# Performance work log

Hardware: AMD Instinct MI355X
Metric: run time of the kernel (lower is better)

The kernel has to match this reference:

```python
import jax, jax.numpy as jnp
import numpy as np

B, T, C, H, N_LAYER, LAYER_ID = 4, 2048, 1024, 16, 12, 6
N = C // H
Q = 256  # T % 256 == 0 -> chunk size used by the module


def setup_inputs():
    key = jax.random.key(0)
    ks = jax.random.split(key, 9)
    r0 = LAYER_ID / (N_LAYER - 1)
    r1 = 1.0 - LAYER_ID / N_LAYER
    ddd = (jnp.arange(C, dtype=jnp.float32) / C)[None, None, :]
    h = jnp.arange(C, dtype=jnp.float32)
    s = 1.0 / np.sqrt(C)
    return {
        "x": jax.random.normal(ks[0], (B, T, C), jnp.float32),
        "time_maa_x": 1.0 - ddd ** r1,
        "time_maa_w": 1.0 - ddd ** r1,
        "time_maa_k": 1.0 - ddd ** r1,
        "time_maa_v": 1.0 - (ddd ** r1 + 0.3 * r0),
        "time_maa_r": 1.0 - ddd ** (0.5 * r1),
        "maa_w1": jax.random.uniform(ks[1], (C, 4 * 32), jnp.float32, minval=-0.01, maxval=0.01),
        "maa_w2": jax.random.uniform(ks[2], (4, 32, C), jnp.float32, minval=-0.01, maxval=0.01),
        "decay_w1": jax.random.uniform(ks[3], (C, 64), jnp.float32, minval=-0.01, maxval=0.01),
        "decay_w2": jax.random.uniform(ks[4], (64, C), jnp.float32, minval=-0.01, maxval=0.01),
        "time_decay": (-6.0 + 5.0 * (h / (C - 1)) ** (0.7 + 1.3 * r0))[None, None, :],
        "time_faaaa": (r0 * (1.0 - h / (C - 1))).reshape(1, H, 1, 1, N),
        "Wr": jax.random.normal(ks[5], (C, C), jnp.float32) * s,
        "Wk": jax.random.normal(ks[6], (C, C), jnp.float32) * s,
        "Wv": jax.random.normal(ks[7], (C, C), jnp.float32) * s,
        "Wo": jax.random.normal(ks[8], (C, C), jnp.float32) * s,
        "ln_g": jnp.ones((C,), jnp.float32),
        "ln_b": jnp.zeros((C,), jnp.float32),
    }


def _forward(x, time_maa_x, time_maa_w, time_maa_k, time_maa_v, time_maa_r,
             maa_w1, maa_w2, decay_w1, decay_w2, time_decay, time_faaaa,
             Wr, Wk, Wv, Wo, ln_g, ln_b):
    b, t, c = x.shape
    nc = t // Q
    # time_shift: zero-pad one step at front of time axis, drop last step
    xx = jnp.pad(x, ((0, 0), (1, 0), (0, 0)))[:, :-1] - x
    xxx = x + xx * time_maa_x
    m = jnp.tanh(xxx @ maa_w1).reshape(b, t, 4, -1)  # [B,T,4,32]
    m = jnp.einsum('btfd,fdc->fbtc', m, maa_w2)       # [4,B,T,C]
    mw, mk, mv, mr = m[0], m[1], m[2], m[3]
    xw = x + xx * (time_maa_w + mw)
    xk = x + xx * (time_maa_k + mk)
    xv = x + xx * (time_maa_v + mv)
    xr = x + xx * (time_maa_r + mr)
    r = (xr @ Wr).reshape(b, t, H, N).transpose(0, 2, 1, 3)  # [B,H,T,N]
    k = (xk @ Wk).reshape(b, t, H, N).transpose(0, 2, 1, 3)
    v = (xv @ Wv).reshape(b, t, H, N).transpose(0, 2, 1, 3)
    w = time_decay + jnp.tanh(xw @ decay_w1) @ decay_w2      # [B,T,C]
    w = w.reshape(b, t, H, N).transpose(0, 2, 1, 3).mean(axis=-1)  # [B,H,T]
    w_log = -jnp.exp(w)
    wc = w_log.reshape(b, H, nc, Q, 1)
    wc_cum = jnp.cumsum(wc, axis=-2)
    shifted = jnp.pad(wc_cum, ((0, 0), (0, 0), (0, 0), (1, 0), (0, 0)))[..., :-1, :]
    ws_log = wc.sum(axis=-2, keepdims=True)   # [B,H,nc,1,1]
    w_inter = jnp.exp(ws_log - wc_cum)        # [B,H,nc,Q,1]
    w_intra = jnp.exp(wc_cum - wc)            # [B,H,nc,Q,1]
    ws = jnp.exp(ws_log)                      # [B,H,nc,1,1]
    A = shifted - jnp.swapaxes(wc_cum, -1, -2)  # [B,H,nc,Q,Q]
    strict = jnp.tril(jnp.ones((Q, Q), dtype=bool), -1)
    # torch: tril() -> exp() -> tril(-1)  ==  exp on strict-lower, zero elsewhere
    w_mask = jnp.where(strict, jnp.exp(jnp.where(strict, A, 0.0)), 0.0)
    rr = r.reshape(b, H, nc, Q, N)
    kk = k.reshape(b, H, nc, Q, N)
    vv = v.reshape(b, H, nc, Q, N)
    kv = jnp.einsum('bhcqn,bhcqm->bhcnm', kk * w_inter, vv)  # [B,H,nc,N,N]

    def step(state, inp):
        ws_i, kv_i = inp
        return ws_i * state + kv_i, state  # emit state BEFORE update (as in torch loop)

    _, states = jax.lax.scan(step, jnp.zeros((b, H, N, N), x.dtype),
                             (jnp.moveaxis(ws, 2, 0), jnp.moveaxis(kv, 2, 0)))
    states = jnp.moveaxis(states, 0, 2)  # [B,H,nc,N,N]
    inter = jnp.einsum('bhcqn,bhcnm->bhcqm', rr * w_intra, states)
    scores = jnp.einsum('bhcqn,bhckn->bhcqk', rr, kk) * w_mask
    diag = jnp.sum(rr * (time_faaaa * kk), axis=-1)  # [B,H,nc,Q]
    intra = jnp.einsum('bhcqk,bhckm->bhcqm', scores, vv) + diag[..., None] * vv
    y = (inter + intra).reshape(b, H, t, N).transpose(0, 2, 1, 3).reshape(b, t, c)
    mu = y.mean(axis=-1, keepdims=True)
    var = ((y - mu) ** 2).mean(axis=-1, keepdims=True)
    y = (y - mu) / jnp.sqrt(var + 1e-5) * ln_g + ln_b  # ln_x
    return y @ Wo  # output projection (dropout p=0)


def reference(x, time_maa_x, time_maa_w, time_maa_k, time_maa_v, time_maa_r,
              maa_w1, maa_w2, decay_w1, decay_w2, time_decay, time_faaaa,
              Wr, Wk, Wv, Wo, ln_g, ln_b):
    return _forward(x, time_maa_x, time_maa_w, time_maa_k, time_maa_v, time_maa_r,
                    maa_w1, maa_w2, decay_w1, decay_w2, time_decay, time_faaaa,
                    Wr, Wk, Wv, Wo, ln_g, ln_b)
```

## Files before the change

### kernel.cpp

```cpp
#include <hip/hip_runtime.h>
#include <math.h>

#define BB 4
#define TT 2048
#define CC 1024
#define HH 16
#define NN 64
#define QQ 256
#define NCH 8
#define BT 8192

typedef unsigned short u16;
typedef __attribute__((ext_vector_type(8))) short bf16x8;
typedef __attribute__((ext_vector_type(4))) short bf16x4;
typedef __attribute__((ext_vector_type(4))) float f32x4;
typedef __attribute__((ext_vector_type(4))) u16 u16x4;

__device__ inline u16 f2b(float x) {
  union { float f; unsigned u; } v;
  v.f = x;
  unsigned r = v.u + 0x7FFFu + ((v.u >> 16) & 1u);
  return (u16)(r >> 16);
}
__device__ inline float b2f(u16 u) {
  union { unsigned u; float f; } v;
  v.u = ((unsigned)u) << 16;
  return v.f;
}
__device__ inline bf16x8 ldfrag(const u16* p) {
  bf16x4 lo = *(const bf16x4*)p;
  bf16x4 hi = *(const bf16x4*)(p + 4);
  return __builtin_shufflevector(lo, hi, 0, 1, 2, 3, 4, 5, 6, 7);
}
__device__ inline void stage_tile(const u16* __restrict__ g, size_t base,
                                  int pitch, int tid, u16* __restrict__ lds) {
#pragma unroll
  for (int it = 0; it < 2; it++) {
    int cidx = tid + it * 256;
    int r = cidx >> 3, c8 = (cidx & 7) * 8;
    bf16x8 v = *(const bf16x8*)(g + base + (size_t)r * pitch + c8);
    *(bf16x4*)(lds + r * 72 + c8) = __builtin_shufflevector(v, v, 0, 1, 2, 3);
    *(bf16x4*)(lds + r * 72 + c8 + 4) = __builtin_shufflevector(v, v, 4, 5, 6, 7);
  }
}

__global__ __launch_bounds__(256) void mix_kernel(const float* __restrict__ x,
                                                  const float* __restrict__ tmx,
                                                  float* __restrict__ xx,
                                                  u16* __restrict__ xxxb) {
  size_t e = ((size_t)blockIdx.x * 256 + threadIdx.x) * 4;
  int c = (int)(e & 1023);
  size_t row = e >> 10;
  int t = (int)(row & 2047);
  float4 xv = *(const float4*)(x + e);
  float4 pv = make_float4(0.f, 0.f, 0.f, 0.f);
  if (t > 0) pv = *(const float4*)(x + e - 1024);
  float4 d = make_float4(pv.x - xv.x, pv.y - xv.y, pv.z - xv.z, pv.w - xv.w);
  *(float4*)(xx + e) = d;
  u16x4 o;
  o.x = f2b(xv.x + d.x * tmx[c + 0]);
  o.y = f2b(xv.y + d.y * tmx[c + 1]);
  o.z = f2b(xv.z + d.z * tmx[c + 2]);
  o.w = f2b(xv.w + d.w * tmx[c + 3]);
  *(u16x4*)(xxxb + e) = o;
}

__global__ __launch_bounds__(256) void cvt_wT(const float* __restrict__ W0,
                                              const float* __restrict__ W1,
                                              const float* __restrict__ W2,
                                              const float* __restrict__ W3,
                                              u16* __restrict__ O0,
                                              u16* __restrict__ O1,
                                              u16* __restrict__ O2,
                                              u16* __restrict__ O3) {
  const float* W;
  u16* O;
  switch (blockIdx.z) {
    case 0: W = W0; O = O0; break;
    case 1: W = W1; O = O1; break;
    case 2: W = W2; O = O2; break;
    default: W = W3; O = O3; break;
  }
  __shared__ float t[64][65];
  int bx = blockIdx.x * 64;
  int by = blockIdx.y * 64;
#pragma unroll
  for (int it = 0; it < 16; it++) {
    int idx = it * 256 + threadIdx.x;
    int r = idx >> 6, c = idx & 63;
    t[r][c] = W[(size_t)(by + r) * 1024 + bx + c];
  }
  __syncthreads();
#pragma unroll
  for (int it = 0; it < 16; it++) {
    int idx = it * 256 + threadIdx.x;
    int n = idx >> 6, k = idx & 63;
    O[(size_t)(bx + n) * 1024 + by + k] = f2b(t[k][n]);
  }
}

__global__ __launch_bounds__(256) void cvt_T(const float* __restrict__ in,
                                             u16* __restrict__ out, int R, int C) {
  __shared__ float t[64][65];
  int c0 = blockIdx.x * 64, r0 = blockIdx.y * 64;
#pragma unroll
  for (int it = 0; it < 16; it++) {
    int idx = it * 256 + threadIdx.x;
    int r = idx >> 6, c = idx & 63;
    t[r][c] = in[(size_t)(r0 + r) * C + c0 + c];
  }
  __syncthreads();
#pragma unroll
  for (int it = 0; it < 16; it++) {
    int idx = it * 256 + threadIdx.x;
    int c = idx >> 6, r = idx & 63;
    out[(size_t)(c0 + c) * R + r0 + r] = f2b(t[r][c]);
  }
}

template <bool TANH>
__global__ __launch_bounds__(256) void gemm_bt_mfma(const u16* __restrict__ A,
                                                    const u16* __restrict__ Bt,
                                                    float* __restrict__ Cf,
                                                    u16* __restrict__ Cb,
                                                    int M, int N, int K) {
  __shared__ u16 As[128 * 32];
  __shared__ u16 Bs[128 * 32];
  const int tid = threadIdx.x;
  const int lane = tid & 63;
  const int row0 = blockIdx.y * 128;
  const int col0 = blockIdx.x * 128;
  const int wave = tid >> 6;
  const int wr = (wave >> 1) * 64;
  const int wc = (wave & 1) * 64;
  const int fr = lane & 15;
  const int fq = lane >> 4;

  f32x4 acc[4][4];
#pragma unroll
  for (int i = 0; i < 4; i++)
#pragma unroll
    for (int j = 0; j < 4; j++) acc[i][j] = (f32x4){0.f, 0.f, 0.f, 0.f};

  const int i0 = tid, i1 = tid + 256;
  const int ra0 = i0 >> 2, ca0 = (i0 & 3) * 8;
  const int ra1 = i1 >> 2, ca1 = (i1 & 3) * 8;

  for (int k0 = 0; k0 < K; k0 += 32) {
    __builtin_amdgcn_global_load_lds(
        (const __attribute__((address_space(1))) void*)(A + (size_t)(row0 + ra0) * K + k0 + ca0),
        (__attribute__((address_space(3))) void*)(As + i0 * 8), 16, 0, 0);
    __builtin_amdgcn_global_load_lds(
        (const __attribute__((address_space(1))) void*)(A + (size_t)(row0 + ra1) * K + k0 + ca1),
        (__attribute__((address_space(3))) void*)(As + i1 * 8), 16, 0, 0);
    __builtin_amdgcn_global_load_lds(
        (const __attribute__((address_space(1))) void*)(Bt + (size_t)(col0 + ra0) * K + k0 + ca0),
        (__attribute__((address_space(3))) void*)(Bs + i0 * 8), 16, 0, 0);
    __builtin_amdgcn_global_load_lds(
        (const __attribute__((address_space(1))) void*)(Bt + (size_t)(col0 + ra1) * K + k0 + ca1),
        (__attribute__((address_space(3))) void*)(Bs + i1 * 8), 16, 0, 0);
    __syncthreads();

    bf16x8 af[4], bf[4];
#pragma unroll
    for (int i = 0; i < 4; i++)
      af[i] = *(const bf16x8*)(As + ((wr + i * 16 + fr) * 32 + fq * 8));
#pragma unroll
    for (int j = 0; j < 4; j++)
      bf[j] = *(const bf16x8*)(Bs + ((wc + j * 16 + fr) * 32 + fq * 8));
#pragma unroll
    for (int i = 0; i < 4; i++)
#pragma unroll
      for (int j = 0; j < 4; j++)
        acc[i][j] = __builtin_amdgcn_mfma_f32_16x16x32_bf16(af[i], bf[j], acc[i][j], 0, 0, 0);
    __syncthreads();
  }
#pragma unroll
  for (int i = 0; i < 4; i++) {
    int grow = row0 + wr + i * 16 + fq * 4;
#pragma unroll
    for (int j = 0; j < 4; j++) {
      int gcol = col0 + wc + j * 16 + fr;
#pragma unroll
      for (int r = 0; r < 4; r++) {
        float vv = acc[i][j][r];
        if (TANH) vv = tanhf(vv);
        if (Cf) Cf[(size_t)(grow + r) * N + gcol] = vv;
        if (Cb) Cb[(size_t)(grow + r) * N + gcol] = f2b(vv);
      }
    }
  }
}

#define DP_ABUF 8192
#define DP_BBUF 16384
#define DP_SBUF 24576
#define DP_SMEM_BYTES 147456

template <bool TRIPLE, bool F32OUT>
__global__ __launch_bounds__(512, 2) void gemm_dp(
    const u16* __restrict__ A0, const u16* __restrict__ A1,
    const u16* __restrict__ A2, const u16* __restrict__ B0,
    const u16* __restrict__ B1, const u16* __restrict__ B2,
    float* __restrict__ Cf, u16* __restrict__ C0, u16* __restrict__ C1,
    u16* __restrict__ C2) {
  extern __shared__ __align__(16) u16 smem[];
  const int nwg = (int)(gridDim.x * gridDim.y * gridDim.z);
  const int wg = (int)(blockIdx.x + (blockIdx.y << 2) + (blockIdx.z << 8));
  const int cpx = nwg >> 3;
  const int swz = (wg & 7) * cpx + (wg >> 3);
  const int bx = swz & 3;
  const int by = (swz >> 2) & 63;
  const int bz = swz >> 8;

  const u16* __restrict__ A;
  const u16* __restrict__ Bt;
  u16* __restrict__ Cb;
  if (TRIPLE) {
    switch (bz) {
      case 0: A = A0; Bt = B0; Cb = C0; break;
      case 1: A = A1; Bt = B1; Cb = C1; break;
      default: A = A2; Bt = B2; Cb = C2; break;
    }
  } else {
    A = A0; Bt = B0; Cb = C0;
  }

  const int tid = threadIdx.x;
  const int lane = tid & 63;
  const int wave = tid >> 6;
  const int wr = (wave >> 2) * 64;
  const int wc = (wave & 3) * 64;
  const int fr = lane & 15;
  const int fq = lane >> 4;
  const int s8 = fr & 7;
  const int row0 = by * 128;
  const int col0 = bx * 256;

  int aoff[4][2], boff[4][2];
#pragma unroll
  for (int mi = 0; mi < 4; mi++)
#pragma unroll
    for (int ks = 0; ks < 2; ks++)
      aoff[mi][ks] = (wr + mi * 16 + fr) * 64 + (((ks * 4 + fq) ^ s8) * 8);
#pragma unroll
  for (int nj = 0; nj < 4; nj++)
#pragma unroll
    for (int ks = 0; ks < 2; ks++)
      boff[nj][ks] = (wc + nj * 16 + fr) * 64 + (((ks * 4 + fq) ^ s8) * 8);

  auto stage = [&](int kt, int q) {
    const u16* __restrict__ gA = A + (size_t)row0 * 1024 + kt * 64;
    const u16* __restrict__ gB = Bt + (size_t)col0 * 1024 + kt * 64;
    u16* dA = smem + q * DP_SBUF;
    u16* dB = dA + DP_ABUF;
#pragma unroll
    for (int p = 0; p < 2; p++) {
      int pos = tid + p * 512;
      int r = pos >> 3, gch = (pos & 7) ^ (r & 7);
      __builtin_amdgcn_global_load_lds(
          (const __attribute__((address_space(1))) void*)(gA + (size_t)r * 1024 + gch * 8),
          (__attribute__((address_space(3))) void*)(dA + pos * 8), 16, 0, 0);
    }
#pragma unroll
    for (int p = 0; p < 4; p++) {
      int pos = tid + p * 512;
      int r = pos >> 3, gch = (pos & 7) ^ (r & 7);
      __builtin_amdgcn_global_load_lds(
          (const __attribute__((address_space(1))) void*)(gB + (size_t)r * 1024 + gch * 8),
          (__attribute__((address_space(3))) void*)(dB + pos * 8), 16, 0, 0);
    }
  };

  f32x4 acc[4][4];
#pragma unroll
  for (int mi = 0; mi < 4; mi++)
#pragma unroll
    for (int nj = 0; nj < 4; nj++) acc[mi][nj] = (f32x4){0.f, 0.f, 0.f, 0.f};

  auto iter_body = [&](int qc, int qs, bool dostage, int t2) {
    if (dostage) stage(t2, qs);
    const u16* sA = smem + qc * DP_SBUF;
    const u16* sB = sA + DP_ABUF;
    bf16x8 av[4][2], bv[4][2];
#pragma unroll
    for (int mi = 0; mi < 4; mi++)
#pragma unroll
      for (int ks = 0; ks < 2; ks++)
        av[mi][ks] = *(const bf16x8*)(sA + aoff[mi][ks]);
#pragma unroll
    for (int nj = 0; nj < 4; nj++)
#pragma unroll
      for (int ks = 0; ks < 2; ks++)
        bv[nj][ks] = *(const bf16x8*)(sB + boff[nj][ks]);
    __builtin_amdgcn_s_setprio(1);
#pragma unroll
    for (int ks = 0; ks < 2; ks++)
#pragma unroll
      for (int mi = 0; mi < 4; mi++)
#pragma unroll
        for (int nj = 0; nj < 4; nj++)
          acc[mi][nj] = __builtin_amdgcn_mfma_f32_16x16x32_bf16(
              av[mi][ks], bv[nj][ks], acc[mi][nj], 0, 0, 0);
    __builtin_amdgcn_s_setprio(0);
  };

  stage(0, 0);
  stage(1, 1);
  int qc = 0, qs = 2;
  for (int t = 0; t < 14; t++) {
    asm volatile("s_waitcnt vmcnt(6)" ::: "memory");
    __builtin_amdgcn_s_barrier();
    iter_body(qc, qs, true, t + 2);
    qc = (qc == 2) ? 0 : qc + 1;
    qs = (qs == 2) ? 0 : qs + 1;
  }
  asm volatile("s_waitcnt vmcnt(6)" ::: "memory");
  __builtin_amdgcn_s_barrier();
  iter_body(qc, 0, false, 0);
  qc = (qc == 2) ? 0 : qc + 1;
  asm volatile("s_waitcnt vmcnt(0)" ::: "memory");
  __builtin_amdgcn_s_barrier();
  iter_body(qc, 0, false, 0);

#pragma unroll
  for (int mi = 0; mi < 4; mi++) {
    int grow = row0 + wr + mi * 16 + fq * 4;
#pragma unroll
    for (int nj = 0; nj < 4; nj++) {
      int gcol = col0 + wc + nj * 16 + fr;
#pragma unroll
      for (int r = 0; r < 4; r++) {
        if (F32OUT)
          Cf[(size_t)(grow + r) * 1024 + gcol] = acc[mi][nj][r];
        else
          Cb[(size_t)(grow + r) * 1024 + gcol] = f2b(acc[mi][nj][r]);
      }
    }
  }
}

__global__ __launch_bounds__(256) void blend_mfma(
    const u16* __restrict__ mb, const u16* __restrict__ w2T,
    const float* __restrict__ x, const float* __restrict__ xx,
    const float* __restrict__ tmw, const float* __restrict__ tmk,
    const float* __restrict__ tmv, const float* __restrict__ tmr,
    u16* __restrict__ xwb, u16* __restrict__ xkb, u16* __restrict__ xvb,
    u16* __restrict__ xrb) {
  __shared__ u16 mS[64 * 136];
  __shared__ u16 wS[64 * 136];
  const int tid = threadIdx.x;
  const int lane = tid & 63;
  const int w = tid >> 6;
  const int fr = lane & 15;
  const int fq = lane >> 4;
  const int c0 = blockIdx.x * 64;
  const int bt0 = blockIdx.y * 64;

#pragma unroll
  for (int it = 0; it < 4; it++) {
    int idx = tid + it * 256;
    int r = idx >> 4, c8 = (idx & 15) * 8;
    bf16x8 v = *(const bf16x8*)(mb + (size_t)(bt0 + r) * 128 + c8);
    *(bf16x4*)(mS + r * 136 + c8) = __builtin_shufflevector(v, v, 0, 1, 2, 3);
    *(bf16x4*)(mS + r * 136 + c8 + 4) = __builtin_shufflevector(v, v, 4, 5, 6, 7);
    bf16x8 u = *(const bf16x8*)(w2T + (size_t)(c0 + r) * 128 + c8);
    *(bf16x4*)(wS + r * 136 + c8) = __builtin_shufflevector(u, u, 0, 1, 2, 3);
    *(bf16x4*)(wS + r * 136 + c8 + 4) = __builtin_shufflevector(u, u, 4, 5, 6, 7);
  }
  __syncthreads();

  f32x4 acc[4][4];
#pragma unroll
  for (int j = 0; j < 4; j++)
#pragma unroll
    for (int f = 0; f < 4; f++) acc[j][f] = (f32x4){0.f, 0.f, 0.f, 0.f};

#pragma unroll
  for (int f = 0; f < 4; f++) {
    bf16x8 aA = ldfrag(mS + (w * 16 + fr) * 136 + f * 32 + fq * 8);
#pragma unroll
    for (int j = 0; j < 4; j++) {
      bf16x8 bB = ldfrag(wS + (j * 16 + fr) * 136 + f * 32 + fq * 8);
      acc[j][f] = __builtin_amdgcn_mfma_f32_16x16x32_bf16(aA, bB, acc[j][f], 0, 0, 0);
    }
  }

#pragma unroll
  for (int j = 0; j < 4; j++) {
    int c = c0 + j * 16 + fr;
    float w_ = tmw[c], k_ = tmk[c], v_ = tmv[c], r_ = tmr[c];
#pragma unroll
    for (int rr = 0; rr < 4; rr++) {
      int bt = bt0 + w * 16 + fq * 4 + rr;
      size_t g = (size_t)bt * 1024 + c;
      float xv_ = x[g], dx = xx[g];
      xwb[g] = f2b(xv_ + dx * (w_ + acc[j][0][rr]));
      xkb[g] = f2b(xv_ + dx * (k_ + acc[j][1][rr]));
      xvb[g] = f2b(xv_ + dx * (v_ + acc[j][2][rr]));
      xrb[g] = f2b(xv_ + dx * (r_ + acc[j][3][rr]));
    }
  }
}

__global__ __launch_bounds__(256) void dw2r_kernel(const float* __restrict__ dw2,
                                                   const float* __restrict__ td,
                                                   float* __restrict__ dw2r,
                                                   float* __restrict__ tdr,
                                                   u16* __restrict__ dw2rbT) {
  int idx = blockIdx.x * 256 + threadIdx.x;
  if (idx < 1024) {
    int j = idx >> 4, h = idx & 15;
    float s = 0.f;
    for (int n = 0; n < 64; n++) s += dw2[(size_t)j * 1024 + h * 64 + n];
    float m = s * (1.f / 64.f);
    dw2r[j * 16 + h] = m;
    dw2rbT[h * 64 + j] = f2b(m);
  }
  if (idx < 16) {
    float s = 0.f;
    for (int n = 0; n < 64; n++) s += td[idx * 64 + n];
    tdr[idx] = s * (1.f / 64.f);
  }
}

__global__ __launch_bounds__(256) void decay_mfma(const u16* __restrict__ xwb,
                                                  const u16* __restrict__ d1T,
                                                  const u16* __restrict__ dw2rbT,
                                                  const float* __restrict__ tdr,
                                                  float* __restrict__ wlog) {
  __shared__ u16 As[64 * 32];
  __shared__ u16 Bs[64 * 32];
  __shared__ u16 h1S[64 * 72];
  __shared__ u16 dwS[16 * 72];
  const int tid = threadIdx.x;
  const int lane = tid & 63;
  const int w = tid >> 6;
  const int fr = lane & 15;
  const int fq = lane >> 4;
  const int bt0 = blockIdx.x * 64;

#pragma unroll
  for (int it = 0; it < 4; it++) {
    int idx = tid + it * 256;
    int r = idx >> 6, c = idx & 63;
    dwS[r * 72 + c] = dw2rbT[r * 64 + c];
  }

  f32x4 acc[4];
#pragma unroll
  for (int j = 0; j < 4; j++) acc[j] = (f32x4){0.f, 0.f, 0.f, 0.f};

  const int ra = tid >> 2, ca = (tid & 3) * 8;
  for (int k0 = 0; k0 < 1024; k0 += 32) {
    __builtin_amdgcn_global_load_lds(
        (const __attribute__((address_space(1))) void*)(xwb + (size_t)(bt0 + ra) * 1024 + k0 + ca),
        (__attribute__((address_space(3))) void*)(As + tid * 8), 16, 0, 0);
    __builtin_amdgcn_global_load_lds(
        (const __attribute__((address_space(1))) void*)(d1T + (size_t)ra * 1024 + k0 + ca),
        (__attribute__((address_space(3))) void*)(Bs + tid * 8), 16, 0, 0);
    __syncthreads();
    bf16x8 aA = *(const bf16x8*)(As + ((w * 16 + fr) * 32 + fq * 8));
#pragma unroll
    for (int j = 0; j < 4; j++) {
      bf16x8 bB = *(const bf16x8*)(Bs + ((j * 16 + fr) * 32 + fq * 8));
      acc[j] = __builtin_amdgcn_mfma_f32_16x16x32_bf16(aA, bB, acc[j], 0, 0, 0);
    }
    __syncthreads();
  }
#pragma unroll
  for (int j = 0; j < 4; j++)
#pragma unroll
    for (int rr = 0; rr < 4; rr++)
      h1S[(w * 16 + fq * 4 + rr) * 72 + j * 16 + fr] = f2b(tanhf(acc[j][rr]));
  __syncthreads();

  f32x4 a2 = (f32x4){0.f, 0.f, 0.f, 0.f};
#pragma unroll
  for (int ks = 0; ks < 2; ks++) {
    bf16x8 aA = ldfrag(h1S + (w * 16 + fr) * 72 + ks * 32 + fq * 8);
    bf16x8 bB = ldfrag(dwS + fr * 72 + ks * 32 + fq * 8);
    a2 = __builtin_amdgcn_mfma_f32_16x16x32_bf16(aA, bB, a2, 0, 0, 0);
  }
  float tdv = tdr[fr];
#pragma unroll
  for (int rr = 0; rr < 4; rr++) {
    int bt = bt0 + w * 16 + fq * 4 + rr;
    int b = bt >> 11, tl = bt & 2047;
    wlog[((size_t)(b * 16 + fr)) * 2048 + tl] = -__expf(tdv + a2[rr]);
  }
}

__global__ __launch_bounds__(256) void wprep_kernel(const float* __restrict__ wlog,
                                                    float* __restrict__ cum,
                                                    float* __restrict__ excl,
                                                    float* __restrict__ wsl) {
  int bid = blockIdx.x;
  int c = bid & 7, bh = bid >> 3;
  int q = threadIdx.x;
  float v = wlog[(size_t)bh * 2048 + c * 256 + q];
  __shared__ float s[256];
  s[q] = v;
  float val = v;
  for (int off = 1; off < 256; off <<= 1) {
    __syncthreads();
    float t = (q >= off) ? s[q - off] : 0.f;
    __syncthreads();
    val += t;
    s[q] = val;
  }
  __syncthreads();
  float total = s[255];
  cum[(size_t)bid * 256 + q] = val;
  excl[(size_t)bid * 256 + q] = val - v;
  if (q == 0) wsl[bid] = total;
}

__global__ __launch_bounds__(256) void kvtrans2_kernel(
    const u16* __restrict__ vb, const u16* __restrict__ kb,
    const u16* __restrict__ rb, const float* __restrict__ faaaa,
    const float* __restrict__ cum, const float* __restrict__ wsl,
    u16* __restrict__ vT, u16* __restrict__ kTw, float* __restrict__ diagG) {
  int tt = blockIdx.x;
  int bh = blockIdx.y;
  int b = bh >> 4, h = bh & 15;
  int cc = tt >> 2;
  int bidc = bh * 8 + cc;
  __shared__ float tv[64][65];
  __shared__ float tk[64][65];
  __shared__ float wfac[64];
  __shared__ float faS[64];
  const int tid = threadIdx.x;
  float wslog = wsl[bidc];
  if (tid < 64) {
    wfac[tid] = __expf(wslog - cum[(size_t)bidc * 256 + (tt & 3) * 64 + tid]);
    faS[tid] = faaaa[h * 64 + tid];
  }
  __syncthreads();
  const int m = tid & 63;
  float fam = faS[m];
#pragma unroll
  for (int it = 0; it < 16; it++) {
    int r = it * 4 + (tid >> 6);
    size_t g = ((size_t)(b * TT + tt * 64 + r)) * CC + h * 64 + m;
    float vraw = b2f(vb[g]);
    float kraw = b2f(kb[g]);
    float rraw = b2f(rb[g]);
    tv[r][m] = vraw;
    tk[r][m] = kraw;
    float s = rraw * fam * kraw;
    s += __shfl_xor(s, 1);
    s += __shfl_xor(s, 2);
    s += __shfl_xor(s, 4);
    s += __shfl_xor(s, 8);
    s += __shfl_xor(s, 16);
    s += __shfl_xor(s, 32);
    if (m == 0) diagG[(size_t)bh * 2048 + tt * 64 + r] = s;
  }
  __syncthreads();
#pragma unroll
  for (int it = 0; it < 16; it++) {
    int idx = it * 256 + tid;
    int mm = idx >> 6, tl = idx & 63;
    size_t o = ((size_t)(bh * 64 + mm)) * TT + tt * 64 + tl;
    vT[o] = f2b(tv[tl][mm]);
    kTw[o] = f2b(tk[tl][mm] * wfac[tl]);
  }
}

__global__ __launch_bounds__(256) void kv_mfma(const u16* __restrict__ kTw,
                                               const u16* __restrict__ vT,
                                               float* __restrict__ kvb) {
  int bid = blockIdx.x;
  int c = bid & 7, bh = bid >> 3;
  __shared__ u16 kS[64 * 72];
  __shared__ u16 vS[64 * 72];
  const int tid = threadIdx.x;
  const int lane = tid & 63;
  const int w = tid >> 6;
  const int fr = lane & 15;
  const int fq = lane >> 4;
  f32x4 acc[4];
#pragma unroll
  for (int j = 0; j < 4; j++) acc[j] = (f32x4){0.f, 0.f, 0.f, 0.f};
  const size_t base = (size_t)bh * 64 * TT + c * QQ;
  for (int qt = 0; qt < 4; qt++) {
    __syncthreads();
    stage_tile(kTw, base + qt * 64, TT, tid, kS);
    stage_tile(vT, base + qt * 64, TT, tid, vS);
    __syncthreads();
#pragma unroll
    for (int ks = 0; ks < 2; ks++) {
      bf16x8 aA = ldfrag(kS + (w * 16 + fr) * 72 + ks * 32 + fq * 8);
#pragma unroll
      for (int j = 0; j < 4; j++) {
        bf16x8 bB = ldfrag(vS + (j * 16 + fr) * 72 + ks * 32 + fq * 8);
        acc[j] = __builtin_amdgcn_mfma_f32_16x16x32_bf16(aA, bB, acc[j], 0, 0, 0);
      }
    }
  }
#pragma unroll
  for (int j = 0; j < 4; j++)
#pragma unroll
    for (int rr = 0; rr < 4; rr++)
      kvb[(size_t)bid * 4096 + (w * 16 + fq * 4 + rr) * 64 + j * 16 + fr] = acc[j][rr];
}

__global__ __launch_bounds__(256) void scan_kernel(const float* __restrict__ kvb,
                                                   const float* __restrict__ wsl,
                                                   float* __restrict__ st) {
  int bh = blockIdx.x;
  int tid = threadIdx.x;
  float s[16];
#pragma unroll
  for (int i = 0; i < 16; i++) s[i] = 0.f;
  for (int c = 0; c < 8; c++) {
    int bid = bh * 8 + c;
    float w = __expf(wsl[bid]);
#pragma unroll
    for (int i = 0; i < 16; i++) {
      size_t e = (size_t)bid * 4096 + i * 256 + tid;
      st[e] = s[i];
      s[i] = w * s[i] + kvb[e];
    }
  }
}

__global__ __launch_bounds__(256) void attn_mfma(
    const u16* __restrict__ rb, const u16* __restrict__ kb,
    const u16* __restrict__ vT, const float* __restrict__ stg,
    const float* __restrict__ cum, const float* __restrict__ excl,
    const float* __restrict__ diagG, float* __restrict__ y) {
  int bid = blockIdx.x;
  int c = bid & 7, bh = bid >> 3;
  int b = bh >> 4, h = bh & 15;
  __shared__ u16 rt[64 * 72];
  __shared__ u16 kt[64 * 72];
  __shared__ u16 vt[64 * 72];
  __shared__ u16 pt[64 * 72];
  __shared__ u16 stT[64 * 72];
  __shared__ float cumS[256], exS[256], diagS[256], ekS[256];

  const int tid = threadIdx.x;
  const int lane = tid & 63;
  const int w = tid >> 6;
  const int fr = lane & 15;
  const int fq = lane >> 4;

  cumS[tid] = cum[(size_t)bid * 256 + tid];
  exS[tid] = excl[(size_t)bid * 256 + tid];
  diagS[tid] = diagG[(size_t)bh * 2048 + c * 256 + tid];
#pragma unroll
  for (int it = 0; it < 16; it++) {
    int idx = tid + it * 256;
    int n = idx >> 6, mm = idx & 63;
    stT[mm * 72 + n] = f2b(stg[(size_t)bid * 4096 + idx]);
  }
  __syncthreads();
  const float ccm = cumS[127];
  ekS[tid] = __expf(ccm - cumS[tid]);

  const size_t rowbase = ((size_t)b * TT + c * QQ) * CC + h * 64;
  const size_t vbase0 = (size_t)bh * 64 * TT + c * QQ;

  for (int qt = 0; qt < 4; qt++) {
    __syncthreads();
    stage_tile(rb, rowbase + (size_t)(qt * 64) * CC, CC, tid, rt);
    __syncthreads();

    f32x4 acc[4];
#pragma unroll
    for (int jm = 0; jm < 4; jm++) acc[jm] = (f32x4){0.f, 0.f, 0.f, 0.f};
    bf16x8 rA[2];
    rA[0] = ldfrag(rt + (w * 16 + fr) * 72 + fq * 8);
    rA[1] = ldfrag(rt + (w * 16 + fr) * 72 + 32 + fq * 8);
#pragma unroll
    for (int ks = 0; ks < 2; ks++)
#pragma unroll
      for (int jm = 0; jm < 4; jm++) {
        bf16x8 bB = ldfrag(stT + (jm * 16 + fr) * 72 + ks * 32 + fq * 8);
        acc[jm] = __builtin_amdgcn_mfma_f32_16x16x32_bf16(rA[ks], bB, acc[jm], 0, 0, 0);
      }
    int ql0 = w * 16 + fq * 4;
    float er[4], eqc[4];
#pragma unroll
    for (int rr = 0; rr < 4; rr++) {
      float ex = exS[qt * 64 + ql0 + rr];
      er[rr] = __expf(ex);
      eqc[rr] = __expf(ex - ccm);
    }
#pragma unroll
    for (int jm = 0; jm < 4; jm++)
#pragma unroll
      for (int rr = 0; rr < 4; rr++) acc[jm][rr] *= er[rr];

    for (int kti = 0; kti <= qt; kti++) {
      __syncthreads();
      stage_tile(kb, rowbase + (size_t)(kti * 64) * CC, CC, tid, kt);
      stage_tile(vT, vbase0 + (size_t)(kti * 64), TT, tid, vt);
      __syncthreads();

      f32x4 sacc[4];
#pragma unroll
      for (int jj = 0; jj < 4; jj++) sacc[jj] = (f32x4){0.f, 0.f, 0.f, 0.f};
#pragma unroll
      for (int ks = 0; ks < 2; ks++)
#pragma unroll
        for (int jj = 0; jj < 4; jj++) {
          bf16x8 bB = ldfrag(kt + (jj * 16 + fr) * 72 + ks * 32 + fq * 8);
          sacc[jj] = __builtin_amdgcn_mfma_f32_16x16x32_bf16(rA[ks], bB, sacc[jj], 0, 0, 0);
        }
#pragma unroll
      for (int jj = 0; jj < 4; jj++) {
        int kcol = kti * 64 + jj * 16 + fr;
        float ek = ekS[kcol];
#pragma unroll
        for (int rr = 0; rr < 4; rr++) {
          int qrow = qt * 64 + ql0 + rr;
          float vsc;
          if (kcol < qrow)
            vsc = sacc[jj][rr] * eqc[rr] * ek;
          else if (kcol == qrow)
            vsc = diagS[qrow];
          else
            vsc = 0.f;
          pt[(ql0 + rr) * 72 + jj * 16 + fr] = f2b(vsc);
        }
      }
      __syncthreads();
#pragma unroll
      for (int ks = 0; ks < 2; ks++) {
        bf16x8 pA = ldfrag(pt + (w * 16 + fr) * 72 + ks * 32 + fq * 8);
#pragma unroll
        for (int jm = 0; jm < 4; jm++) {
          bf16x8 vB = ldfrag(vt + (jm * 16 + fr) * 72 + ks * 32 + fq * 8);
          acc[jm] = __builtin_amdgcn_mfma_f32_16x16x32_bf16(pA, vB, acc[jm], 0, 0, 0);
        }
      }
    }
    int qg0 = qt * 64 + w * 16 + fq * 4;
#pragma unroll
    for (int jm = 0; jm < 4; jm++)
#pragma unroll
      for (int rr = 0; rr < 4; rr++)
        y[rowbase + (size_t)(qg0 + rr) * CC + jm * 16 + fr] = acc[jm][rr];
  }
}

__global__ __launch_bounds__(256) void ln_kernel(const float* __restrict__ y,
                                                 const float* __restrict__ g,
                                                 const float* __restrict__ bta,
                                                 u16* __restrict__ out) {
  __shared__ float red[8];
  int bt = blockIdx.x;
  int tid = threadIdx.x;
  float v[4];
  float s = 0.f;
#pragma unroll
  for (int i = 0; i < 4; i++) {
    v[i] = y[(size_t)bt * 1024 + i * 256 + tid];
    s += v[i];
  }
#pragma unroll
  for (int off = 32; off > 0; off >>= 1) s += __shfl_down(s, off);
  if ((tid & 63) == 0) red[tid >> 6] = s;
  __syncthreads();
  if (tid == 0) red[4] = red[0] + red[1] + red[2] + red[3];
  __syncthreads();
  float mu = red[4] * (1.f / 1024.f);
  float s2 = 0.f;
#pragma unroll
  for (int i = 0; i < 4; i++) {
    float d = v[i] - mu;
    s2 += d * d;
  }
#pragma unroll
  for (int off = 32; off > 0; off >>= 1) s2 += __shfl_down(s2, off);
  __syncthreads();
  if ((tid & 63) == 0) red[tid >> 6] = s2;
  __syncthreads();
  if (tid == 0) red[5] = red[0] + red[1] + red[2] + red[3];
  __syncthreads();
  float var = red[5] * (1.f / 1024.f);
  float rstd = rsqrtf(var + 1e-5f);
#pragma unroll
  for (int i = 0; i < 4; i++) {
    int c = i * 256 + tid;
    out[(size_t)bt * 1024 + c] = f2b((v[i] - mu) * rstd * g[c] + bta[c]);
  }
}

extern "C" void kernel_launch(void* const* d_in, const int* in_sizes, int n_in,
                              void* d_out, int out_size, void* d_ws,
                              size_t ws_size, hipStream_t stream) {
  const float* x = (const float*)d_in[0];
  const float* tmx = (const float*)d_in[1];
  const float* tmw = (const float*)d_in[2];
  const float* tmk = (const float*)d_in[3];
  const float* tmv = (const float*)d_in[4];
  const float* tmr = (const float*)d_in[5];
  const float* maa_w1 = (const float*)d_in[6];
  const float* maa_w2 = (const float*)d_in[7];
  const float* decay_w1 = (const float*)d_in[8];
  const float* decay_w2 = (const float*)d_in[9];
  const float* time_decay = (const float*)d_in[10];
  const float* faaaa = (const float*)d_in[11];
  const float* Wr = (const float*)d_in[12];
  const float* Wk = (const float*)d_in[13];
  const float* Wv = (const float*)d_in[14];
  const float* Wo = (const float*)d_in[15];
  const float* lng = (const float*)d_in[16];
  const float* lnb = (const float*)d_in[17];
  float* out = (float*)d_out;
  float* ws = (float*)d_ws;

  const size_t S = (size_t)BT * CC;

  float* xx = ws;
  float* dw2r = ws + S;
  float* tdr = dw2r + 1024;
  float* wlog = tdr + 1024;
  float* cum = wlog + 131072;
  float* excl = cum + 131072;
  float* wsl = excl + 131072;
  float* diagG = wsl + 1024;
  float* kvb = diagG + 131072;
  float* stb = kvb + (size_t)512 * 4096;
  float* fend = stb + (size_t)512 * 4096;
  u16* xxxb = (u16*)fend;
  u16* mb = xxxb + S;
  u16* xkb = mb + (size_t)BT * 128;
  u16* xvb = xkb + S;
  u16* xrb = xvb + S;
  u16* xwb = xrb + S;
  u16* rb16 = xwb + S;
  u16* kb16 = rb16 + S;
  u16* Vb = kb16 + S;
  u16* Wrt = Vb + S;
  u16* Wkt = Wrt + (size_t)1024 * 1024;
  u16* Wvt = Wkt + (size_t)1024 * 1024;
  u16* Wot = Wvt + (size_t)1024 * 1024;
  u16* w1T = Wot + (size_t)1024 * 1024;
  u16* w2T = w1T + (size_t)128 * 1024;
  u16* d1T = w2T + (size_t)1024 * 128;
  u16* dw2rbT = d1T + (size_t)64 * 1024;
  u16* vT = xxxb;
  u16* kTw = xrb;
  float* y_ = xx;
  u16* ylnb = xkb;

  static bool attr_done = false;
  if (!attr_done) {
    hipFuncSetAttribute((const void*)gemm_dp<true, false>,
                        hipFuncAttributeMaxDynamicSharedMemorySize, DP_SMEM_BYTES);
    hipFuncSetAttribute((const void*)gemm_dp<false, true>,
                        hipFuncAttributeMaxDynamicSharedMemorySize, DP_SMEM_BYTES);
    attr_done = true;
  }

  cvt_wT<<<dim3(16, 16, 4), 256, 0, stream>>>(Wr, Wk, Wv, Wo, Wrt, Wkt, Wvt, Wot);
  cvt_T<<<dim3(2, 16), 256, 0, stream>>>(maa_w1, w1T, 1024, 128);
  cvt_T<<<dim3(16, 2), 256, 0, stream>>>(maa_w2, w2T, 128, 1024);
  cvt_T<<<dim3(1, 16), 256, 0, stream>>>(decay_w1, d1T, 1024, 64);
  dw2r_kernel<<<4, 256, 0, stream>>>(decay_w2, time_decay, dw2r, tdr, dw2rbT);
  mix_kernel<<<8192, 256, 0, stream>>>(x, tmx, xx, xxxb);
  gemm_bt_mfma<true><<<dim3(1, 64), 256, 0, stream>>>(xxxb, w1T, nullptr, mb, BT, 128, CC);
  blend_mfma<<<dim3(16, 128), 256, 0, stream>>>(mb, w2T, x, xx, tmw, tmk, tmv,
                                                tmr, xwb, xkb, xvb, xrb);
  decay_mfma<<<128, 256, 0, stream>>>(xwb, d1T, dw2rbT, tdr, wlog);
  wprep_kernel<<<512, 256, 0, stream>>>(wlog, cum, excl, wsl);
  gemm_dp<true, false><<<dim3(4, 64, 3), 512, DP_SMEM_BYTES, stream>>>(
      xrb, xkb, xvb, Wrt, Wkt, Wvt, nullptr, rb16, kb16, Vb);
  kvtrans2_kernel<<<dim3(32, 64), 256, 0, stream>>>(Vb, kb16, rb16, faaaa, cum,
                                                    wsl, vT, kTw, diagG);
  kv_mfma<<<512, 256, 0, stream>>>(kTw, vT, kvb);
  scan_kernel<<<64, 256, 0, stream>>>(kvb, wsl, stb);
  attn_mfma<<<512, 256, 0, stream>>>(rb16, kb16, vT, stb, cum, excl, diagG, y_);
  ln_kernel<<<BT, 256, 0, stream>>>(y_, lng, lnb, ylnb);
  gemm_dp<false, true><<<dim3(4, 64, 1), 512, DP_SMEM_BYTES, stream>>>(
      ylnb, nullptr, nullptr, Wot, nullptr, nullptr, out, nullptr, nullptr,
      nullptr);
}
```

Baseline: 378.5 us.

## Split GEMM k-tile into two ping-pong phases with interleaved staging and barriers

Restructures the gemm_dp main loop so each 64-wide k-tile runs as two half-phases. Each phase loads its LDS fragments, issues part of the next tile's global-to-LDS loads, waits on a barrier and lgkmcnt, then runs 16 MFMAs at raised priority. The aim is to interleave LDS reads, async global loads and MFMA work across the two waves per SIMD, in the style of a ping-pong schedule. The cost is twice as many workgroup barriers per tile and tighter coupling between waves. The vmcnt accounting also has to stay correct now that loads are split across two phases.

```diff
diff --git a/kernel.cpp b/kernel.cpp
--- a/kernel.cpp
+++ b/kernel.cpp
@@ -197,6 +197,11 @@
 #define DP_SBUF 24576
 #define DP_SMEM_BYTES 147456
 
+#define PE_PLAIN 0
+#define PE_VM6 1
+#define PE_VM0 2
+#define PE_NONE 3
+
 template <bool TRIPLE, bool F32OUT>
 __global__ __launch_bounds__(512, 2) void gemm_dp(
     const u16* __restrict__ A0, const u16* __restrict__ A1,
@@ -249,7 +254,7 @@
     for (int ks = 0; ks < 2; ks++)
       boff[nj][ks] = (wc + nj * 16 + fr) * 64 + (((ks * 4 + fq) ^ s8) * 8);
 
-  auto stage = [&](int kt, int q) {
+  auto stage_pA = [&](int kt, int q) {
     const u16* __restrict__ gA = A + (size_t)row0 * 1024 + kt * 64;
     const u16* __restrict__ gB = Bt + (size_t)col0 * 1024 + kt * 64;
     u16* dA = smem + q * DP_SBUF;
@@ -262,8 +267,19 @@
           (const __attribute__((address_space(1))) void*)(gA + (size_t)r * 1024 + gch * 8),
           (__attribute__((address_space(3))) void*)(dA + pos * 8), 16, 0, 0);
     }
-#pragma unroll
-    for (int p = 0; p < 4; p++) {
+    {
+      int pos = tid;
+      int r = pos >> 3, gch = (pos & 7) ^ (r & 7);
+      __builtin_amdgcn_global_load_lds(
+          (const __attribute__((address_space(1))) void*)(gB + (size_t)r * 1024 + gch * 8),
+          (__attribute__((address_space(3))) void*)(dB + pos * 8), 16, 0, 0);
+    }
+  };
+  auto stage_pB = [&](int kt, int q) {
+    const u16* __restrict__ gB = Bt + (size_t)col0 * 1024 + kt * 64;
+    u16* dB = smem + q * DP_SBUF + DP_ABUF;
+#pragma unroll
+    for (int p = 1; p < 4; p++) {
       int pos = tid + p * 512;
       int r = pos >> 3, gch = (pos & 7) ^ (r & 7);
       __builtin_amdgcn_global_load_lds(
@@ -278,50 +294,57 @@
 #pragma unroll
     for (int nj = 0; nj < 4; nj++) acc[mi][nj] = (f32x4){0.f, 0.f, 0.f, 0.f};
 
-  auto iter_body = [&](int qc, int qs, bool dostage, int t2) {
-    if (dostage) stage(t2, qs);
+  auto phase = [&](int qc, int ks, int dostage, int t2, int qs, int pe) {
     const u16* sA = smem + qc * DP_SBUF;
     const u16* sB = sA + DP_ABUF;
-    bf16x8 av[4][2], bv[4][2];
+    bf16x8 av[4], bv[4];
+#pragma unroll
+    for (int mi = 0; mi < 4; mi++) av[mi] = *(const bf16x8*)(sA + aoff[mi][ks]);
+#pragma unroll
+    for (int nj = 0; nj < 4; nj++) bv[nj] = *(const bf16x8*)(sB + boff[nj][ks]);
+    if (dostage == 1) stage_pA(t2, qs);
+    else if (dostage == 2) stage_pB(t2, qs);
+    __builtin_amdgcn_s_barrier();
+    asm volatile("s_waitcnt lgkmcnt(0)" ::: "memory");
+    __builtin_amdgcn_sched_barrier(0);
+    __builtin_amdgcn_s_setprio(1);
 #pragma unroll
     for (int mi = 0; mi < 4; mi++)
 #pragma unroll
-      for (int ks = 0; ks < 2; ks++)
-        av[mi][ks] = *(const bf16x8*)(sA + aoff[mi][ks]);
-#pragma unroll
-    for (int nj = 0; nj < 4; nj++)
-#pragma unroll
-      for (int ks = 0; ks < 2; ks++)
-        bv[nj][ks] = *(const bf16x8*)(sB + boff[nj][ks]);
-    __builtin_amdgcn_s_setprio(1);
-#pragma unroll
-    for (int ks = 0; ks < 2; ks++)
-#pragma unroll
-      for (int mi = 0; mi < 4; mi++)
-#pragma unroll
-        for (int nj = 0; nj < 4; nj++)
-          acc[mi][nj] = __builtin_amdgcn_mfma_f32_16x16x32_bf16(
-              av[mi][ks], bv[nj][ks], acc[mi][nj], 0, 0, 0);
+      for (int nj = 0; nj < 4; nj++)
+        acc[mi][nj] = __builtin_amdgcn_mfma_f32_16x16x32_bf16(
+            av[mi], bv[nj], acc[mi][nj], 0, 0, 0);
     __builtin_amdgcn_s_setprio(0);
+    if (pe == PE_VM6) {
+      asm volatile("s_waitcnt vmcnt(6)" ::: "memory");
+      __builtin_amdgcn_s_barrier();
+    } else if (pe == PE_VM0) {
+      asm volatile("s_waitcnt vmcnt(0)" ::: "memory");
+      __builtin_amdgcn_s_barrier();
+    } else if (pe == PE_PLAIN) {
+      __builtin_amdgcn_s_barrier();
+    }
   };
 
-  stage(0, 0);
-  stage(1, 1);
+  stage_pA(0, 0);
+  stage_pB(0, 0);
+  stage_pA(1, 1);
+  stage_pB(1, 1);
+  asm volatile("s_waitcnt vmcnt(6)" ::: "memory");
+  __builtin_amdgcn_s_barrier();
+
   int qc = 0, qs = 2;
   for (int t = 0; t < 14; t++) {
-    asm volatile("s_waitcnt vmcnt(6)" ::: "memory");
-    __builtin_amdgcn_s_barrier();
-    iter_body(qc, qs, true, t + 2);
+    phase(qc, 0, 1, t + 2, qs, PE_PLAIN);
+    phase(qc, 1, 2, t + 2, qs, PE_VM6);
     qc = (qc == 2) ? 0 : qc + 1;
     qs = (qs == 2) ? 0 : qs + 1;
   }
-  asm volatile("s_waitcnt vmcnt(6)" ::: "memory");
-  __builtin_amdgcn_s_barrier();
-  iter_body(qc, 0, false, 0);
+  phase(qc, 0, 0, 0, 0, PE_PLAIN);
+  phase(qc, 1, 0, 0, 0, PE_VM0);
   qc = (qc == 2) ? 0 : qc + 1;
-  asm volatile("s_waitcnt vmcnt(0)" ::: "memory");
-  __builtin_amdgcn_s_barrier();
-  iter_body(qc, 0, false, 0);
+  phase(qc, 0, 0, 0, 0, PE_PLAIN);
+  phase(qc, 1, 0, 0, 0, PE_NONE);
 
 #pragma unroll
   for (int mi = 0; mi < 4; mi++) {
```

After: 387.7 us. +2.5%, slower.

## Use 4-wave 128x64-per-wave tiles in projection GEMM with reordered staging

Applied to the files above, without the earlier changes.

The projection GEMM drops from 8 waves of 64x64 warp tiles to 4 waves, each computing a 128x64 tile. Each wave then holds a 32-accumulator register tile and reuses its B fragments across more rows, so it issues fewer LDS reads per MFMA. The next-tile global-to-LDS prefetch is moved after the fragment loads, and the wait plus barrier moves to the end of each iteration. The cost is fewer waves to hide latency and much higher register pressure, with one block per CU given the launch bounds.

```diff
diff --git a/kernel.cpp b/kernel.cpp
--- a/kernel.cpp
+++ b/kernel.cpp
@@ -197,8 +197,12 @@
 #define DP_SBUF 24576
 #define DP_SMEM_BYTES 147456
 
+#define TE_VM12 0
+#define TE_VM0 1
+#define TE_NONE 2
+
 template <bool TRIPLE, bool F32OUT>
-__global__ __launch_bounds__(512, 2) void gemm_dp(
+__global__ __launch_bounds__(256, 1) void gemm_dp(
     const u16* __restrict__ A0, const u16* __restrict__ A1,
     const u16* __restrict__ A2, const u16* __restrict__ B0,
     const u16* __restrict__ B1, const u16* __restrict__ B2,
@@ -229,20 +233,19 @@
   const int tid = threadIdx.x;
   const int lane = tid & 63;
   const int wave = tid >> 6;
-  const int wr = (wave >> 2) * 64;
-  const int wc = (wave & 3) * 64;
+  const int wc = wave * 64;
   const int fr = lane & 15;
   const int fq = lane >> 4;
   const int s8 = fr & 7;
   const int row0 = by * 128;
   const int col0 = bx * 256;
 
-  int aoff[4][2], boff[4][2];
-#pragma unroll
-  for (int mi = 0; mi < 4; mi++)
+  int aoff[8][2], boff[4][2];
+#pragma unroll
+  for (int mi = 0; mi < 8; mi++)
 #pragma unroll
     for (int ks = 0; ks < 2; ks++)
-      aoff[mi][ks] = (wr + mi * 16 + fr) * 64 + (((ks * 4 + fq) ^ s8) * 8);
+      aoff[mi][ks] = (mi * 16 + fr) * 64 + (((ks * 4 + fq) ^ s8) * 8);
 #pragma unroll
   for (int nj = 0; nj < 4; nj++)
 #pragma unroll
@@ -255,16 +258,16 @@
     u16* dA = smem + q * DP_SBUF;
     u16* dB = dA + DP_ABUF;
 #pragma unroll
-    for (int p = 0; p < 2; p++) {
-      int pos = tid + p * 512;
+    for (int p = 0; p < 4; p++) {
+      int pos = tid + p * 256;
       int r = pos >> 3, gch = (pos & 7) ^ (r & 7);
       __builtin_amdgcn_global_load_lds(
           (const __attribute__((address_space(1))) void*)(gA + (size_t)r * 1024 + gch * 8),
           (__attribute__((address_space(3))) void*)(dA + pos * 8), 16, 0, 0);
     }
 #pragma unroll
-    for (int p = 0; p < 4; p++) {
-      int pos = tid + p * 512;
+    for (int p = 0; p < 8; p++) {
+      int pos = tid + p * 256;
       int r = pos >> 3, gch = (pos & 7) ^ (r & 7);
       __builtin_amdgcn_global_load_lds(
           (const __attribute__((address_space(1))) void*)(gB + (size_t)r * 1024 + gch * 8),
@@ -272,60 +275,68 @@
     }
   };
 
-  f32x4 acc[4][4];
-#pragma unroll
-  for (int mi = 0; mi < 4; mi++)
+  f32x4 acc[8][4];
+#pragma unroll
+  for (int mi = 0; mi < 8; mi++)
 #pragma unroll
     for (int nj = 0; nj < 4; nj++) acc[mi][nj] = (f32x4){0.f, 0.f, 0.f, 0.f};
 
-  auto iter_body = [&](int qc, int qs, bool dostage, int t2) {
-    if (dostage) stage(t2, qs);
+  auto body = [&](int qc, bool dostage, int t2, int qs, int te) {
     const u16* sA = smem + qc * DP_SBUF;
     const u16* sB = sA + DP_ABUF;
-    bf16x8 av[4][2], bv[4][2];
-#pragma unroll
-    for (int mi = 0; mi < 4; mi++)
-#pragma unroll
-      for (int ks = 0; ks < 2; ks++)
-        av[mi][ks] = *(const bf16x8*)(sA + aoff[mi][ks]);
-#pragma unroll
-    for (int nj = 0; nj < 4; nj++)
-#pragma unroll
-      for (int ks = 0; ks < 2; ks++)
-        bv[nj][ks] = *(const bf16x8*)(sB + boff[nj][ks]);
+    bf16x8 a0[8], b0[4], a1[8], b1[4];
+#pragma unroll
+    for (int mi = 0; mi < 8; mi++) a0[mi] = *(const bf16x8*)(sA + aoff[mi][0]);
+#pragma unroll
+    for (int nj = 0; nj < 4; nj++) b0[nj] = *(const bf16x8*)(sB + boff[nj][0]);
+#pragma unroll
+    for (int mi = 0; mi < 8; mi++) a1[mi] = *(const bf16x8*)(sA + aoff[mi][1]);
+#pragma unroll
+    for (int nj = 0; nj < 4; nj++) b1[nj] = *(const bf16x8*)(sB + boff[nj][1]);
+    if (dostage) stage(t2, qs);
     __builtin_amdgcn_s_setprio(1);
 #pragma unroll
-    for (int ks = 0; ks < 2; ks++)
-#pragma unroll
-      for (int mi = 0; mi < 4; mi++)
-#pragma unroll
-        for (int nj = 0; nj < 4; nj++)
-          acc[mi][nj] = __builtin_amdgcn_mfma_f32_16x16x32_bf16(
-              av[mi][ks], bv[nj][ks], acc[mi][nj], 0, 0, 0);
+    for (int mi = 0; mi < 8; mi++)
+#pragma unroll
+      for (int nj = 0; nj < 4; nj++)
+        acc[mi][nj] = __builtin_amdgcn_mfma_f32_16x16x32_bf16(
+            a0[mi], b0[nj], acc[mi][nj], 0, 0, 0);
     __builtin_amdgcn_s_setprio(0);
+    __builtin_amdgcn_s_setprio(1);
+#pragma unroll
+    for (int mi = 0; mi < 8; mi++)
+#pragma unroll
+      for (int nj = 0; nj < 4; nj++)
+        acc[mi][nj] = __builtin_amdgcn_mfma_f32_16x16x32_bf16(
+            a1[mi], b1[nj], acc[mi][nj], 0, 0, 0);
+    __builtin_amdgcn_s_setprio(0);
+    if (te == TE_VM12) {
+      asm volatile("s_waitcnt vmcnt(12)" ::: "memory");
+      __builtin_amdgcn_s_barrier();
+    } else if (te == TE_VM0) {
+      asm volatile("s_waitcnt vmcnt(0)" ::: "memory");
+      __builtin_amdgcn_s_barrier();
+    }
   };
 
   stage(0, 0);
   stage(1, 1);
+  asm volatile("s_waitcnt vmcnt(12)" ::: "memory");
+  __builtin_amdgcn_s_barrier();
+
   int qc = 0, qs = 2;
   for (int t = 0; t < 14; t++) {
-    asm volatile("s_waitcnt vmcnt(6)" ::: "memory");
-    __builtin_amdgcn_s_barrier();
-    iter_body(qc, qs, true, t + 2);
+    body(qc, true, t + 2, qs, TE_VM12);
     qc = (qc == 2) ? 0 : qc + 1;
     qs = (qs == 2) ? 0 : qs + 1;
   }
-  asm volatile("s_waitcnt vmcnt(6)" ::: "memory");
-  __builtin_amdgcn_s_barrier();
-  iter_body(qc, 0, false, 0);
+  body(qc, false, 0, 0, TE_VM0);
   qc = (qc == 2) ? 0 : qc + 1;
-  asm volatile("s_waitcnt vmcnt(0)" ::: "memory");
-  __builtin_amdgcn_s_barrier();
-  iter_body(qc, 0, false, 0);
-
-#pragma unroll
-  for (int mi = 0; mi < 4; mi++) {
-    int grow = row0 + wr + mi * 16 + fq * 4;
+  body(qc, false, 0, 0, TE_NONE);
+
+#pragma unroll
+  for (int mi = 0; mi < 8; mi++) {
+    int grow = row0 + mi * 16 + fq * 4;
 #pragma unroll
     for (int nj = 0; nj < 4; nj++) {
       int gcol = col0 + wc + nj * 16 + fr;
@@ -869,7 +880,7 @@
                                                 tmr, xwb, xkb, xvb, xrb);
   decay_mfma<<<128, 256, 0, stream>>>(xwb, d1T, dw2rbT, tdr, wlog);
   wprep_kernel<<<512, 256, 0, stream>>>(wlog, cum, excl, wsl);
-  gemm_dp<true, false><<<dim3(4, 64, 3), 512, DP_SMEM_BYTES, stream>>>(
+  gemm_dp<true, false><<<dim3(4, 64, 3), 256, DP_SMEM_BYTES, stream>>>(
       xrb, xkb, xvb, Wrt, Wkt, Wvt, nullptr, rb16, kb16, Vb);
   kvtrans2_kernel<<<dim3(32, 64), 256, 0, stream>>>(Vb, kb16, rb16, faaaa, cum,
                                                     wsl, vT, kTw, diagG);
@@ -877,7 +888,7 @@
   scan_kernel<<<64, 256, 0, stream>>>(kvb, wsl, stb);
   attn_mfma<<<512, 256, 0, stream>>>(rb16, kb16, vT, stb, cum, excl, diagG, y_);
   ln_kernel<<<BT, 256, 0, stream>>>(y_, lng, lnb, ylnb);
-  gemm_dp<false, true><<<dim3(4, 64, 1), 512, DP_SMEM_BYTES, stream>>>(
+  gemm_dp<false, true><<<dim3(4, 64, 1), 256, DP_SMEM_BYTES, stream>>>(
       ylnb, nullptr, nullptr, Wot, nullptr, nullptr, out, nullptr, nullptr,
       nullptr);
 }
```

New measurement: 404.7 us. 6.9% more time.
